# Performance work log

Hardware: AMD Instinct MI355X
Metric: run time of the kernel (lower is better)

The kernel has to match this reference:

```python
import jax, jax.numpy as jnp
import numpy as np

DIM = 1024
NUM_HEADS = 16
HEAD_DIM = DIM // NUM_HEADS


def setup_inputs() -> dict:
    key = jax.random.key(0)
    ks = jax.random.split(key, 9)
    s = 1.0 / np.sqrt(DIM)
    return {
        "x": jax.random.normal(ks[0], (2, 2048, DIM), dtype=jnp.float32),
        "wq": jax.random.uniform(ks[1], (DIM, DIM), jnp.float32, -s, s),
        "bq": jax.random.uniform(ks[2], (DIM,), jnp.float32, -s, s),
        "wk": jax.random.uniform(ks[3], (DIM, DIM), jnp.float32, -s, s),
        "bk": jax.random.uniform(ks[4], (DIM,), jnp.float32, -s, s),
        "wv": jax.random.uniform(ks[5], (DIM, DIM), jnp.float32, -s, s),
        "bv": jax.random.uniform(ks[6], (DIM,), jnp.float32, -s, s),
        "wo": jax.random.uniform(ks[7], (DIM, DIM), jnp.float32, -s, s),
        "bo": jax.random.uniform(ks[8], (DIM,), jnp.float32, -s, s),
    }


def reference(x, wq, bq, wk, bk, wv, bv, wo, bo):
    B, N, D = x.shape
    H, Hd = NUM_HEADS, HEAD_DIM
    # projections; weights stored as (in, out) so x @ w matches torch Linear(x) with w = W.T
    q = (x @ wq + bq).reshape(B, N, H, Hd).transpose(0, 2, 1, 3)  # [B,H,N,Hd]
    k = (x @ wk + bk).reshape(B, N, H, Hd).transpose(0, 2, 1, 3)
    v = (x @ wv + bv).reshape(B, N, H, Hd).transpose(0, 2, 1, 3)
    scale = 1.0 / np.sqrt(Hd).astype(np.float32)
    scores = jnp.einsum("bhqd,bhkd->bhqk", q, k) * scale  # [B,H,N,N]
    attn = jax.nn.softmax(scores, axis=-1)
    # dropout is identity in eval mode (reference baseline)
    out = jnp.einsum("bhqk,bhkd->bhqd", attn, v)  # [B,H,N,Hd]
    out = out.transpose(0, 2, 1, 3).reshape(B, N, D)
    return out @ wo + bo
```

## Files before the change

### kernel.cpp

```cpp
#include <hip/hip_runtime.h>

typedef __attribute__((ext_vector_type(8))) short short8;
typedef __attribute__((ext_vector_type(4))) short short4v;
typedef __attribute__((ext_vector_type(4))) float f32x4;

__device__ inline unsigned short f2bf(float f) {
  union { float f; unsigned int u; } v; v.f = f;
  unsigned int r = v.u + 0x7FFFu + ((v.u >> 16) & 1u);
  return (unsigned short)(r >> 16);
}

__device__ inline unsigned cvtpk_bf16(float lo, float hi) {
  unsigned r;
  asm("v_cvt_pk_bf16_f32 %0, %1, %2" : "=v"(r) : "v"(lo), "v"(hi));
  return r;
}

__device__ inline void gload_lds16(const void* g, void* l) {
  __builtin_amdgcn_global_load_lds(
      (const __attribute__((address_space(1))) unsigned int*)g,
      (__attribute__((address_space(3))) unsigned int*)l, 16, 0, 0);
}


__global__ __launch_bounds__(256) void prep(
    const float* __restrict__ x,
    const float* __restrict__ wq, const float* __restrict__ wk,
    const float* __restrict__ wv, const float* __restrict__ wo,
    const float* __restrict__ bq, const float* __restrict__ bk,
    const float* __restrict__ bv,
    unsigned short* __restrict__ xb, unsigned short* __restrict__ wqkvT,
    unsigned short* __restrict__ woT, float* __restrict__ bqkv) {
  const int bid = blockIdx.x;
  if (bid < 4096) {
    const int i = bid * 256 + threadIdx.x;
    float4 v = ((const float4*)x)[i];
    ushort4 o;
    o.x = f2bf(v.x); o.y = f2bf(v.y); o.z = f2bf(v.z); o.w = f2bf(v.w);
    ((ushort4*)xb)[i] = o;
  } else if (bid < 8192) {
    const int u = bid - 4096;
    const int z = u >> 10, rem = u & 1023;
    const float* w = (z == 0) ? wq : (z == 1) ? wk : (z == 2) ? wv : wo;
    unsigned short* dst = (z < 3) ? (wqkvT + (size_t)z * 1024 * 1024) : woT;
    const float scale = (z == 0) ? 0.18033688011f : 1.0f;
    __shared__ float t[32][33];
    const int k0 = (rem & 31) * 32;
    const int n0 = (rem >> 5) * 32;
    const int tx = threadIdx.x & 31, ty = threadIdx.x >> 5;
#pragma unroll
    for (int i = 0; i < 32; i += 8)
      t[ty + i][tx] = w[(size_t)(k0 + ty + i) * 1024 + n0 + tx];
    __syncthreads();
#pragma unroll
    for (int i = 0; i < 32; i += 8)
      dst[(size_t)(n0 + ty + i) * 1024 + k0 + tx] = f2bf(t[tx][ty + i] * scale);
  } else {
    const int i = (bid - 8192) * 256 + threadIdx.x;
    float v;
    if (i < 1024) v = bq[i] * 0.18033688011f;
    else if (i < 2048) v = bk[i - 1024];
    else v = bv[i - 2048];
    bqkv[i] = v;
  }
}


__global__ __launch_bounds__(256) void gemm_bt64b(
    const unsigned short* __restrict__ A, const unsigned short* __restrict__ Bt,
    const float* __restrict__ bias, float* __restrict__ C, int K, int ldc) {
  __shared__ unsigned short As[64 * 32];
  __shared__ unsigned short Bs[64 * 32];
  const int tid = threadIdx.x;
  const int lane = tid & 63;
  const int wave = tid >> 6;
  const int wm = (wave >> 1) * 32;
  const int wn = (wave & 1) * 32;
  const long bm = (long)blockIdx.x * 64;
  const long bn = (long)blockIdx.y * 64;

  const int sr = tid >> 2;
  const int sc = (tid & 3) * 8;
  const unsigned short* Ag0 = A + (bm + sr) * (long)K + sc;
  const unsigned short* Bg0 = Bt + (bn + sr) * (long)K + sc;
  unsigned short* As0 = &As[tid * 8];
  unsigned short* Bs0 = &Bs[tid * 8];

  f32x4 acc[2][2] = {};

  const int fr = lane & 15;
  const int fk = (lane >> 4) * 8;

  for (int kt = 0; kt < K; kt += 32) {
    gload_lds16(Ag0, As0);
    gload_lds16(Bg0, Bs0);
    Ag0 += 32; Bg0 += 32;
    __syncthreads();
    short8 af[2], bfv[2];
#pragma unroll
    for (int i = 0; i < 2; i++) af[i] = *(const short8*)&As[(wm + i * 16 + fr) * 32 + fk];
#pragma unroll
    for (int j = 0; j < 2; j++) bfv[j] = *(const short8*)&Bs[(wn + j * 16 + fr) * 32 + fk];
#pragma unroll
    for (int i = 0; i < 2; i++)
#pragma unroll
      for (int j = 0; j < 2; j++)
        acc[i][j] = __builtin_amdgcn_mfma_f32_16x16x32_bf16(af[i], bfv[j], acc[i][j], 0, 0, 0);
    __syncthreads();
  }

  const int crow = (lane >> 4) * 4;
  const int ccol = lane & 15;
#pragma unroll
  for (int j = 0; j < 2; j++) {
    const long col = bn + wn + j * 16 + ccol;
    const float bv = bias[col];
#pragma unroll
    for (int i = 0; i < 2; i++)
#pragma unroll
      for (int r = 0; r < 4; r++) {
        const long row = bm + wm + i * 16 + crow + r;
        C[row * ldc + col] = acc[i][j][r] + bv;
      }
  }
}


__global__ __launch_bounds__(512, 2) void gemm256(
    const unsigned short* __restrict__ A, const unsigned short* __restrict__ Bt,
    const float* __restrict__ bias, unsigned short* __restrict__ C, int ldc) {
  constexpr int K = 1024;
  __shared__ unsigned short Sab[2][2][16384];
  const int tid = threadIdx.x;
  const int lane = tid & 63;
  const int w = tid >> 6;
  const int wr = w >> 2, wc = w & 3;
  const long bm = (long)blockIdx.x * 256;
  const long bn = (long)blockIdx.y * 256;
  const int fr = lane & 15, fg = lane >> 4;

  const int srow = tid >> 3;
  const int kch = tid & 7;

  auto stage = [&](int o, int buf, int tk, int h) {
#pragma unroll
    for (int l = 0; l < 2; ++l) {
      const int rih = l * 64 + srow;
      const unsigned short* src = (o ? Bt : A) +
          ((o ? bn : bm) + h * 128 + rih) * (long)K + tk * 64 + ((kch ^ (rih & 7)) * 8);
      gload_lds16(src, &Sab[buf][o][h * 8192 + (l * 512 + tid) * 8]);
    }
  };

  f32x4 acc[8][4] = {};

  stage(0, 0, 0, 0); stage(0, 0, 0, 1);
  stage(1, 0, 0, 0); stage(1, 0, 0, 1);
  stage(1, 1, 1, 0); stage(1, 1, 1, 1);
  asm volatile("s_waitcnt vmcnt(4)" ::: "memory");
  __builtin_amdgcn_s_barrier();

  for (int it = 0; it < 8; ++it) {
    const int T = 2 * it;
    const int tkA = (T + 2 < 15) ? T + 2 : 15;
    const int tkB3 = (T + 3 < 15) ? T + 3 : 15;
#pragma unroll
    for (int half = 0; half < 2; ++half) {
      const int b = half;
      short8 bfr[4][2];
      short8 afr[2][2];
#pragma unroll
      for (int g = 0; g < 4; ++g) {
        if (g == 0) {
#pragma unroll
          for (int nj = 0; nj < 4; ++nj)
#pragma unroll
            for (int kc = 0; kc < 2; ++kc) {
              const int r = wc * 64 + nj * 16 + fr;
              bfr[nj][kc] = *(const short8*)&Sab[b][1][r * 64 + ((kc * 4 + fg) ^ (r & 7)) * 8];
            }
        }
#pragma unroll
        for (int mil = 0; mil < 2; ++mil)
#pragma unroll
          for (int kc = 0; kc < 2; ++kc) {
            const int r = wr * 128 + (2 * g + mil) * 16 + fr;
            afr[mil][kc] = *(const short8*)&Sab[b][0][r * 64 + ((kc * 4 + fg) ^ (r & 7)) * 8];
          }
        if (half == 0) {
          if (g == 0)      { stage(0, 1, T + 1, 0); stage(0, 1, T + 1, 1); }
          else if (g == 1) { stage(1, 0, tkA, 0); }
          else if (g == 2) { stage(1, 0, tkA, 1); }
        } else {
          if (g == 0)      { stage(0, 0, tkA, 0); stage(0, 0, tkA, 1); }
          else if (g == 1) { stage(1, 1, tkB3, 0); }
          else if (g == 2) { stage(1, 1, tkB3, 1); }
        }
        __builtin_amdgcn_s_barrier();
        asm volatile("s_waitcnt lgkmcnt(0)" ::: "memory");
        __builtin_amdgcn_sched_barrier(0);
        __builtin_amdgcn_s_setprio(1);
#pragma unroll
        for (int mil = 0; mil < 2; ++mil)
#pragma unroll
          for (int nj = 0; nj < 4; ++nj)
#pragma unroll
            for (int kc = 0; kc < 2; ++kc)
              acc[2 * g + mil][nj] = __builtin_amdgcn_mfma_f32_16x16x32_bf16(
                  afr[mil][kc], bfr[nj][kc], acc[2 * g + mil][nj], 0, 0, 0);
        __builtin_amdgcn_s_setprio(0);
        if (g == 3) asm volatile("s_waitcnt vmcnt(4)" ::: "memory");
        __builtin_amdgcn_s_barrier();
      }
    }
  }

  const int crow = fg * 4;
  const int ccol = fr;
#pragma unroll
  for (int nj = 0; nj < 4; ++nj) {
    const long col = bn + wc * 64 + nj * 16 + ccol;
    const float bv = bias[col];
#pragma unroll
    for (int mi = 0; mi < 8; ++mi)
#pragma unroll
      for (int r = 0; r < 4; ++r) {
        const long row = bm + wr * 128 + mi * 16 + crow + r;
        C[row * ldc + col] = f2bf(acc[mi][nj][r] + bv);
      }
  }
}


#define KSWZ(row) (((row) & 3) | ((((row) >> 3) & 1) << 2))
#define TRRD(d, o) asm volatile("ds_read_b64_tr_b16 %0, %1 offset:" o \
                                : "=v"(d) : "v"(vtr) : "memory")
#define LGKM(n) asm volatile("s_waitcnt lgkmcnt(" #n ")" ::: "memory")

__global__ __launch_bounds__(512, 2) void attn_fwd(
    const unsigned short* __restrict__ qkv, unsigned short* __restrict__ out) {
  __shared__ unsigned short S[6 * 4096];
  __shared__ float msArr[512];
  unsigned short* Ks = &S[0];
  unsigned short* Vs = &S[3 * 4096];
  const int tid = threadIdx.x;
  const int lane = tid & 63;
  const int w = tid >> 6;
  const int qh = w >> 1, kh = w & 1;

  const int xcd = blockIdx.x & 7, slot = blockIdx.x >> 3;
  const int pair = xcd * 4 + (slot >> 4);
  const int qtile = slot & 15;
  const int h = pair & 15, b = pair >> 4;
  const long rowbase = (long)b * 2048;
  const int hq = h * 64;
  const int fr = lane & 15;
  const int fg = lane >> 4;
  const int fk = fg * 8;
  const int q0 = qtile * 128 + qh * 32;

  short8 qf[2][2];
#pragma unroll
  for (int qi = 0; qi < 2; qi++) {
    const long qr = rowbase + q0 + qi * 16 + fr;
    qf[qi][0] = *(const short8*)&qkv[qr * 3072 + hq + fk];
    qf[qi][1] = *(const short8*)&qkv[qr * 3072 + hq + 32 + fk];
  }

  const int kr = tid >> 3;
  const unsigned short* Kg0 = &qkv[(rowbase + kr) * 3072 + 1024 + hq + (((tid & 7) ^ KSWZ(kr)) * 8)];
  const int vkv = ((tid >> 1) & 3) + ((tid >> 5) & 1) * 4 + ((tid >> 3) & 3) * 8 + ((tid >> 8) & 1) * 32;
  const int vd0 = (tid & 1) * 8 + ((tid >> 6) & 3) * 16;
  const unsigned short* Vg0 = &qkv[(rowbase + vkv) * 3072 + 2048 + hq + vd0];

  auto stage = [&](int tk, int buf) {
    const long off = (long)tk * 64 * 3072;
    gload_lds16(Kg0 + off, &Ks[buf * 4096 + tid * 8]);
    gload_lds16(Vg0 + off, &Vs[buf * 4096 + tid * 8]);
  };

  f32x4 o[2][4] = {};
  float m_[2] = {-1e30f, -1e30f};
  float s_[2] = {0.f, 0.f};

  const int krowbase = kh * 32 + (fr >> 2) * 8 + (fr & 3);

  stage(0, 0);
  stage(1, 1);
  asm volatile("s_waitcnt vmcnt(2)" ::: "memory");
  __builtin_amdgcn_s_barrier();

  int cur = 0;

  for (int t = 0; t < 32; t++) {
    {
      int stg = cur + 2; if (stg >= 3) stg -= 3;
      const int tk = (t + 2 < 31) ? t + 2 : 31;
      stage(tk, stg);
    }

    f32x4 sa[2][2];
    __builtin_amdgcn_s_setprio(1);
#pragma unroll
    for (int n = 0; n < 2; n++) {
      const int row = krowbase + n * 4;
      const short8 kf0 = *(const short8*)&Ks[cur * 4096 + ((row * 64 + fk) ^ (KSWZ(row) << 3))];
      const short8 kf1 = *(const short8*)&Ks[cur * 4096 + ((row * 64 + 32 + fk) ^ (KSWZ(row) << 3))];
#pragma unroll
      for (int qi = 0; qi < 2; qi++) {
        f32x4 z = {0.f, 0.f, 0.f, 0.f};
        z = __builtin_amdgcn_mfma_f32_16x16x32_bf16(kf0, qf[qi][0], z, 0, 0, 0);
        sa[qi][n] = __builtin_amdgcn_mfma_f32_16x16x32_bf16(kf1, qf[qi][1], z, 0, 0, 0);
      }
    }
    __builtin_amdgcn_s_setprio(0);

    float lmax[2];
#pragma unroll
    for (int qi = 0; qi < 2; qi++)
      lmax[qi] = fmaxf(fmaxf(fmaxf(sa[qi][0][0], sa[qi][0][1]), fmaxf(sa[qi][0][2], sa[qi][0][3])),
                       fmaxf(fmaxf(sa[qi][1][0], sa[qi][1][1]), fmaxf(sa[qi][1][2], sa[qi][1][3])));
    if (__any(fmaxf(lmax[0] - m_[0], lmax[1] - m_[1]) > 8.f)) {
#pragma unroll
      for (int qi = 0; qi < 2; qi++) {
        float mx = lmax[qi];
        mx = fmaxf(mx, __shfl_xor(mx, 16));
        mx = fmaxf(mx, __shfl_xor(mx, 32));
        const float nm = fmaxf(m_[qi], mx);
        const float fac = __builtin_amdgcn_exp2f(m_[qi] - nm);
        m_[qi] = nm;
        s_[qi] *= fac;
        float facp[4];
#pragma unroll
        for (int r = 0; r < 4; r++) facp[r] = __shfl(fac, fg * 4 + r);
#pragma unroll
        for (int dj = 0; dj < 4; dj++)
#pragma unroll
          for (int r = 0; r < 4; r++) o[qi][dj][r] *= facp[r];
      }
    }

    short8 pa[2];
#pragma unroll
    for (int qi = 0; qi < 2; qi++) {
      float p[8];
#pragma unroll
      for (int n = 0; n < 2; n++)
#pragma unroll
        for (int r = 0; r < 4; r++)
          p[n * 4 + r] = __builtin_amdgcn_exp2f(sa[qi][n][r] - m_[qi]);
      s_[qi] += ((p[0] + p[1]) + (p[2] + p[3])) + ((p[4] + p[5]) + (p[6] + p[7]));
      union { unsigned u[4]; short8 v; } pk;
      pk.u[0] = cvtpk_bf16(p[0], p[1]);
      pk.u[1] = cvtpk_bf16(p[2], p[3]);
      pk.u[2] = cvtpk_bf16(p[4], p[5]);
      pk.u[3] = cvtpk_bf16(p[6], p[7]);
      pa[qi] = pk.v;
    }

    const __attribute__((address_space(3))) unsigned short* vtr =
        (const __attribute__((address_space(3))) unsigned short*)&Vs[0] +
        cur * 4096 + kh * 2048 + lane * 4;
    short4v v0[4], v1[4];
    TRRD(v0[0], "0");    TRRD(v1[0], "512");
    TRRD(v0[1], "1024"); TRRD(v1[1], "1536");
    TRRD(v0[2], "2048"); TRRD(v1[2], "2560");
    TRRD(v0[3], "3072"); TRRD(v1[3], "3584");

    __builtin_amdgcn_s_setprio(1);
    LGKM(6); __builtin_amdgcn_sched_barrier(0);
    {
      short8 vf = __builtin_shufflevector(v0[0], v1[0], 0, 1, 2, 3, 4, 5, 6, 7);
      o[0][0] = __builtin_amdgcn_mfma_f32_16x16x32_bf16(pa[0], vf, o[0][0], 0, 0, 0);
      o[1][0] = __builtin_amdgcn_mfma_f32_16x16x32_bf16(pa[1], vf, o[1][0], 0, 0, 0);
    }
    LGKM(4); __builtin_amdgcn_sched_barrier(0);
    {
      short8 vf = __builtin_shufflevector(v0[1], v1[1], 0, 1, 2, 3, 4, 5, 6, 7);
      o[0][1] = __builtin_amdgcn_mfma_f32_16x16x32_bf16(pa[0], vf, o[0][1], 0, 0, 0);
      o[1][1] = __builtin_amdgcn_mfma_f32_16x16x32_bf16(pa[1], vf, o[1][1], 0, 0, 0);
    }
    LGKM(2); __builtin_amdgcn_sched_barrier(0);
    {
      short8 vf = __builtin_shufflevector(v0[2], v1[2], 0, 1, 2, 3, 4, 5, 6, 7);
      o[0][2] = __builtin_amdgcn_mfma_f32_16x16x32_bf16(pa[0], vf, o[0][2], 0, 0, 0);
      o[1][2] = __builtin_amdgcn_mfma_f32_16x16x32_bf16(pa[1], vf, o[1][2], 0, 0, 0);
    }
    LGKM(0); __builtin_amdgcn_sched_barrier(0);
    {
      short8 vf = __builtin_shufflevector(v0[3], v1[3], 0, 1, 2, 3, 4, 5, 6, 7);
      o[0][3] = __builtin_amdgcn_mfma_f32_16x16x32_bf16(pa[0], vf, o[0][3], 0, 0, 0);
      o[1][3] = __builtin_amdgcn_mfma_f32_16x16x32_bf16(pa[1], vf, o[1][3], 0, 0, 0);
    }
    __builtin_amdgcn_s_setprio(0);

    asm volatile("s_waitcnt vmcnt(2) lgkmcnt(0)" ::: "memory");
    __builtin_amdgcn_s_barrier();

    cur = (cur == 2) ? 0 : cur + 1;
  }

#pragma unroll
  for (int qi = 0; qi < 2; qi++) {
    s_[qi] += __shfl_xor(s_[qi], 16);
    s_[qi] += __shfl_xor(s_[qi], 32);
  }

  float* mo = (float*)&S[0];
  __syncthreads();
  if (kh == 1) {
#pragma unroll
    for (int qi = 0; qi < 2; qi++)
#pragma unroll
      for (int dj = 0; dj < 4; dj++)
#pragma unroll
        for (int r = 0; r < 4; r++)
          mo[(qh * 32 + qi * 16 + dj * 4 + r) * 64 + lane] = o[qi][dj][r];
  }
  if (fg == 0) {
#pragma unroll
    for (int qi = 0; qi < 2; qi++) {
      msArr[(((kh * 4 + qh) * 2 + qi) * 2 + 0) * 16 + fr] = m_[qi];
      msArr[(((kh * 4 + qh) * 2 + qi) * 2 + 1) * 16 + fr] = s_[qi];
    }
  }
  __syncthreads();
  if (kh == 0) {
#pragma unroll
    for (int qi = 0; qi < 2; qi++) {
      float f0[4], f1[4], rs[4];
#pragma unroll
      for (int r = 0; r < 4; r++) {
        const int qp = fg * 4 + r;
        const float m0 = msArr[(((0 * 4 + qh) * 2 + qi) * 2 + 0) * 16 + qp];
        const float s0 = msArr[(((0 * 4 + qh) * 2 + qi) * 2 + 1) * 16 + qp];
        const float m1 = msArr[(((1 * 4 + qh) * 2 + qi) * 2 + 0) * 16 + qp];
        const float s1 = msArr[(((1 * 4 + qh) * 2 + qi) * 2 + 1) * 16 + qp];
        const float mstar = fmaxf(m0, m1);
        f0[r] = __builtin_amdgcn_exp2f(m0 - mstar);
        f1[r] = __builtin_amdgcn_exp2f(m1 - mstar);
        rs[r] = __builtin_amdgcn_rcpf(s0 * f0[r] + s1 * f1[r]);
      }
#pragma unroll
      for (int dj = 0; dj < 4; dj++)
#pragma unroll
        for (int r = 0; r < 4; r++) {
          const float o1 = mo[(qh * 32 + qi * 16 + dj * 4 + r) * 64 + lane];
          const float val = (o[qi][dj][r] * f0[r] + o1 * f1[r]) * rs[r];
          const long row = rowbase + q0 + qi * 16 + fg * 4 + r;
          out[row * 1024 + hq + dj * 16 + fr] = f2bf(val);
        }
    }
  }
}


extern "C" void kernel_launch(void* const* d_in, const int* in_sizes, int n_in,
                              void* d_out, int out_size, void* d_ws, size_t ws_size,
                              hipStream_t stream) {
  const float* x  = (const float*)d_in[0];
  const float* wq = (const float*)d_in[1];
  const float* bq = (const float*)d_in[2];
  const float* wk = (const float*)d_in[3];
  const float* bk = (const float*)d_in[4];
  const float* wv = (const float*)d_in[5];
  const float* bv = (const float*)d_in[6];
  const float* wo = (const float*)d_in[7];
  const float* bo = (const float*)d_in[8];

  char* ws = (char*)d_ws;
  unsigned short* xb    = (unsigned short*)(ws);
  unsigned short* wqkvT = (unsigned short*)(ws + (8ull  << 20));
  unsigned short* woT   = (unsigned short*)(ws + (14ull << 20));
  float*          bqkv  = (float*)         (ws + (16ull << 20));
  unsigned short* qkv   = (unsigned short*)(ws + (17ull << 20));
  unsigned short* attn  = (unsigned short*)(ws + (41ull << 20));

  prep<<<8204, 256, 0, stream>>>(x, wq, wk, wv, wo, bq, bk, bv, xb, wqkvT, woT, bqkv);

  gemm256<<<dim3(16, 12), 512, 0, stream>>>(xb, wqkvT, bqkv, qkv, 3072);

  attn_fwd<<<512, 512, 0, stream>>>(qkv, attn);

  gemm_bt64b<<<dim3(64, 16), 256, 0, stream>>>(attn, woT, bo, (float*)d_out, 1024, 1024);
}
```

Measured before the change: 113.1 us.

## Double-buffer small GEMM LDS tiles and prefetch A fragments one phase ahead

In the 64x64 GEMM, LDS tiles become double-buffered so the next K-slice is issued before the current slice's MFMAs run. In the large GEMM, A-operand fragments for the next phase are read from LDS one group early. The full lgkmcnt(0) wait is relaxed to lgkmcnt(4) for the first three phases, so LDS reads overlap MFMA work. Holding extra fragment registers raises register pressure, which may hurt scheduling or occupancy.

```diff
diff --git a/kernel.cpp b/kernel.cpp
--- a/kernel.cpp
+++ b/kernel.cpp
@@ -21,6 +21,8 @@
       (const __attribute__((address_space(1))) unsigned int*)g,
       (__attribute__((address_space(3))) unsigned int*)l, 16, 0, 0);
 }
+
+#define LGKM(n) asm volatile("s_waitcnt lgkmcnt(" #n ")" ::: "memory")
 
 
 __global__ __launch_bounds__(256) void prep(
@@ -69,8 +71,8 @@
 __global__ __launch_bounds__(256) void gemm_bt64b(
     const unsigned short* __restrict__ A, const unsigned short* __restrict__ Bt,
     const float* __restrict__ bias, float* __restrict__ C, int K, int ldc) {
-  __shared__ unsigned short As[64 * 32];
-  __shared__ unsigned short Bs[64 * 32];
+  __shared__ unsigned short As[2][64 * 32];
+  __shared__ unsigned short Bs[2][64 * 32];
   const int tid = threadIdx.x;
   const int lane = tid & 63;
   const int wave = tid >> 6;
@@ -83,24 +85,30 @@
   const int sc = (tid & 3) * 8;
   const unsigned short* Ag0 = A + (bm + sr) * (long)K + sc;
   const unsigned short* Bg0 = Bt + (bn + sr) * (long)K + sc;
-  unsigned short* As0 = &As[tid * 8];
-  unsigned short* Bs0 = &Bs[tid * 8];
+
+  auto stage = [&](int buf) {
+    gload_lds16(Ag0, &As[buf][tid * 8]);
+    gload_lds16(Bg0, &Bs[buf][tid * 8]);
+    Ag0 += 32; Bg0 += 32;
+  };
 
   f32x4 acc[2][2] = {};
 
   const int fr = lane & 15;
   const int fk = (lane >> 4) * 8;
 
-  for (int kt = 0; kt < K; kt += 32) {
-    gload_lds16(Ag0, As0);
-    gload_lds16(Bg0, Bs0);
-    Ag0 += 32; Bg0 += 32;
-    __syncthreads();
+  stage(0);
+  __syncthreads();
+
+  const int nkt = K / 32;
+  for (int kt = 0; kt < nkt; kt++) {
+    const int cur = kt & 1;
+    if (kt + 1 < nkt) stage(cur ^ 1);
     short8 af[2], bfv[2];
 #pragma unroll
-    for (int i = 0; i < 2; i++) af[i] = *(const short8*)&As[(wm + i * 16 + fr) * 32 + fk];
-#pragma unroll
-    for (int j = 0; j < 2; j++) bfv[j] = *(const short8*)&Bs[(wn + j * 16 + fr) * 32 + fk];
+    for (int i = 0; i < 2; i++) af[i] = *(const short8*)&As[cur][(wm + i * 16 + fr) * 32 + fk];
+#pragma unroll
+    for (int j = 0; j < 2; j++) bfv[j] = *(const short8*)&Bs[cur][(wn + j * 16 + fr) * 32 + fk];
 #pragma unroll
     for (int i = 0; i < 2; i++)
 #pragma unroll
@@ -168,7 +176,7 @@
     for (int half = 0; half < 2; ++half) {
       const int b = half;
       short8 bfr[4][2];
-      short8 afr[2][2];
+      short8 afr[4][2][2];
 #pragma unroll
       for (int g = 0; g < 4; ++g) {
         if (g == 0) {
@@ -179,14 +187,24 @@
               const int r = wc * 64 + nj * 16 + fr;
               bfr[nj][kc] = *(const short8*)&Sab[b][1][r * 64 + ((kc * 4 + fg) ^ (r & 7)) * 8];
             }
+#pragma unroll
+          for (int ph = 0; ph < 2; ++ph)
+#pragma unroll
+            for (int mil = 0; mil < 2; ++mil)
+#pragma unroll
+              for (int kc = 0; kc < 2; ++kc) {
+                const int r = wr * 128 + (2 * ph + mil) * 16 + fr;
+                afr[ph][mil][kc] = *(const short8*)&Sab[b][0][r * 64 + ((kc * 4 + fg) ^ (r & 7)) * 8];
+              }
+        } else if (g < 3) {
+#pragma unroll
+          for (int mil = 0; mil < 2; ++mil)
+#pragma unroll
+            for (int kc = 0; kc < 2; ++kc) {
+              const int r = wr * 128 + (2 * (g + 1) + mil) * 16 + fr;
+              afr[g + 1][mil][kc] = *(const short8*)&Sab[b][0][r * 64 + ((kc * 4 + fg) ^ (r & 7)) * 8];
+            }
         }
-#pragma unroll
-        for (int mil = 0; mil < 2; ++mil)
-#pragma unroll
-          for (int kc = 0; kc < 2; ++kc) {
-            const int r = wr * 128 + (2 * g + mil) * 16 + fr;
-            afr[mil][kc] = *(const short8*)&Sab[b][0][r * 64 + ((kc * 4 + fg) ^ (r & 7)) * 8];
-          }
         if (half == 0) {
           if (g == 0)      { stage(0, 1, T + 1, 0); stage(0, 1, T + 1, 1); }
           else if (g == 1) { stage(1, 0, tkA, 0); }
@@ -197,7 +215,7 @@
           else if (g == 2) { stage(1, 1, tkB3, 1); }
         }
         __builtin_amdgcn_s_barrier();
-        asm volatile("s_waitcnt lgkmcnt(0)" ::: "memory");
+        if (g < 3) { LGKM(4); } else { LGKM(0); }
         __builtin_amdgcn_sched_barrier(0);
         __builtin_amdgcn_s_setprio(1);
 #pragma unroll
@@ -207,7 +225,7 @@
 #pragma unroll
             for (int kc = 0; kc < 2; ++kc)
               acc[2 * g + mil][nj] = __builtin_amdgcn_mfma_f32_16x16x32_bf16(
-                  afr[mil][kc], bfr[nj][kc], acc[2 * g + mil][nj], 0, 0, 0);
+                  afr[g][mil][kc], bfr[nj][kc], acc[2 * g + mil][nj], 0, 0, 0);
         __builtin_amdgcn_s_setprio(0);
         if (g == 3) asm volatile("s_waitcnt vmcnt(4)" ::: "memory");
         __builtin_amdgcn_s_barrier();
@@ -235,7 +253,6 @@
 #define KSWZ(row) (((row) & 3) | ((((row) >> 3) & 1) << 2))
 #define TRRD(d, o) asm volatile("ds_read_b64_tr_b16 %0, %1 offset:" o \
                                 : "=v"(d) : "v"(vtr) : "memory")
-#define LGKM(n) asm volatile("s_waitcnt lgkmcnt(" #n ")" ::: "memory")
 
 __global__ __launch_bounds__(512, 2) void attn_fwd(
     const unsigned short* __restrict__ qkv, unsigned short* __restrict__ out) {
```

New measurement: 119.5 us. 5.7% more time.
